# Optimization experiments

Hardware: AMD Instinct MI355X
Metric: run time of the kernel (lower is better)

## Reference

```python
import jax, jax.numpy as jnp
import numpy as np

B, S, E, H, W = 1, 4096, 1024, 16, 256
D = E // H
SCALE = D ** -0.5


def setup_inputs() -> dict:
    key = jax.random.key(0)
    k1, k2, k3 = jax.random.split(key, 3)
    x = jax.random.normal(k1, (B, S, E), dtype=jnp.float32)
    # torch Linear weight is [out,in]; we store transposed [in,out] so y = x @ w
    w_qkv = jax.random.normal(k2, (E, 3 * E), dtype=jnp.float32) * (E ** -0.5)
    w_out = jax.random.normal(k3, (E, E), dtype=jnp.float32) * (E ** -0.5)
    # sliding-window causal mask: key j allowed for query i iff i-W < j <= i
    q_idx = jnp.arange(S)[:, None]
    k_idx = jnp.arange(S)[None, :]
    allowed_mask = (k_idx <= q_idx) & (k_idx > q_idx - W)  # [S,S] bool
    allowed_mask = allowed_mask[None, None]  # [1,1,S,S]
    return {"x": x, "allowed_mask": allowed_mask, "w_qkv": w_qkv, "w_out": w_out}


def reference(x, allowed_mask, w_qkv, w_out):
    b, s, e = x.shape
    qkv = (x @ w_qkv).reshape(b, s, 3, H, D)
    q, k, v = jnp.moveaxis(qkv, 2, 0)  # each [b,s,H,D]
    q = q.transpose(0, 2, 1, 3)  # [b,H,s,D]
    k = k.transpose(0, 2, 1, 3)
    v = v.transpose(0, 2, 1, 3)
    scores = jnp.einsum('bhsd,bhtd->bhst', q, k) * SCALE  # [b,H,s,s]
    scores = jnp.where(allowed_mask, scores, -jnp.inf)
    attn = jax.nn.softmax(scores, axis=-1)
    out = jnp.einsum('bhst,bhtd->bhsd', attn, v)  # [b,H,s,D]
    out = out.transpose(0, 2, 1, 3).reshape(b, s, e)
    return out @ w_out
```

## Files before the change

### kernel.cpp

```cpp
#include <hip/hip_runtime.h>
#include <hip/hip_bf16.h>

#define S_LEN 4096
#define EMB   1024
#define NH    16
#define HD    64
#define WIN   256
#define SCALE 0.125f

typedef __attribute__((ext_vector_type(8))) short short8;
typedef __attribute__((ext_vector_type(4))) float f32x4;
typedef __attribute__((ext_vector_type(4))) unsigned short us4;

__device__ inline unsigned short f2b(float x) {
    __hip_bfloat16 b = __float2bfloat16(x);
    return *reinterpret_cast<unsigned short*>(&b);
}

__device__ inline void gld_lds16(const unsigned short* g, unsigned short* l) {
    __builtin_amdgcn_global_load_lds(
        (const __attribute__((address_space(1))) unsigned int*)g,
        (__attribute__((address_space(3))) unsigned int*)l,
        16, 0, 0);
}

__device__ inline void transpose_tile(const float* __restrict__ in,
                                      unsigned short* __restrict__ out,
                                      int R, int C, int bx, int by,
                                      unsigned short* t) {
    const int tid = threadIdx.x;
    const int r0 = by * 64, c0 = bx * 64;

    const int rr = tid >> 4, cc = (tid & 15) * 4;
    #pragma unroll
    for (int i = 0; i < 4; ++i) {
        float4 v = *reinterpret_cast<const float4*>(&in[(size_t)(r0 + rr + i * 16) * C + c0 + cc]);
        t[(cc + 0) * 72 + rr + i * 16] = f2b(v.x);
        t[(cc + 1) * 72 + rr + i * 16] = f2b(v.y);
        t[(cc + 2) * 72 + rr + i * 16] = f2b(v.z);
        t[(cc + 3) * 72 + rr + i * 16] = f2b(v.w);
    }
    __syncthreads();

    const int wr = tid >> 2, wk = (tid & 3) * 16;
    #pragma unroll
    for (int p = 0; p < 2; ++p)
        *reinterpret_cast<uint4*>(&out[(size_t)(c0 + wr) * R + r0 + wk + p * 8]) =
            *reinterpret_cast<const uint4*>(&t[wr * 72 + wk + p * 8]);
}

__global__ __launch_bounds__(256) void prep(const float* __restrict__ x,
                                            unsigned short* __restrict__ xb,
                                            const float* __restrict__ w_qkv,
                                            unsigned short* __restrict__ wqkvT,
                                            const float* __restrict__ w_out,
                                            unsigned short* __restrict__ woutT) {
    __shared__ alignas(16) unsigned short t[64 * 72];
    const int b = blockIdx.x;
    if (b < 768) {
        transpose_tile(w_qkv, wqkvT, EMB, 3 * EMB, b % 48, b / 48, t);
    } else if (b < 1024) {
        const int bb = b - 768;
        transpose_tile(w_out, woutT, EMB, EMB, bb & 15, bb >> 4, t);
    } else {
        const size_t tt = (size_t)(b - 1024) * 256 + threadIdx.x;
        const float4* s4 = reinterpret_cast<const float4*>(x) + tt * 4;
        float4 v0 = s4[0], v1 = s4[1], v2 = s4[2], v3 = s4[3];
        us4 p0 = {f2b(v0.x), f2b(v0.y), f2b(v0.z), f2b(v0.w)};
        us4 p1 = {f2b(v1.x), f2b(v1.y), f2b(v1.z), f2b(v1.w)};
        us4 p2 = {f2b(v2.x), f2b(v2.y), f2b(v2.z), f2b(v2.w)};
        us4 p3 = {f2b(v3.x), f2b(v3.y), f2b(v3.z), f2b(v3.w)};
        us4* d = reinterpret_cast<us4*>(xb) + tt * 4;
        d[0] = p0; d[1] = p1; d[2] = p2; d[3] = p3;
    }
}

template <int MODE, int BN>
__global__ __launch_bounds__(256) void gemm_bt(const unsigned short* __restrict__ A,
                                               const unsigned short* __restrict__ Bt,
                                               void* __restrict__ Cout,
                                               unsigned short* __restrict__ vT,
                                               int M, int N, int K) {
    constexpr int SMEM_ELEMS = (MODE == 1) ? 17408 : 8192 + BN * 64;
    constexpr int NJ = BN / 32;
    __shared__ alignas(16) unsigned short smem[SMEM_ELEMS];
    unsigned short* As = smem;
    unsigned short* Bs = smem + 8192;

    const int tid  = threadIdx.x;
    const int lane = tid & 63;
    const int w    = tid >> 6;
    const int quad = lane >> 4;
    const int l16  = lane & 15;

    const int m0 = blockIdx.y * 128;
    const int n0 = blockIdx.x * BN;
    const int m_off = (w & 1) * 64;
    const int n_off = (w >> 1) * (BN / 2);

    const int s_row = tid >> 3;
    const int s_c0  = tid & 7;

    f32x4 acc[4][NJ];
    #pragma unroll
    for (int i = 0; i < 4; ++i)
        #pragma unroll
        for (int j = 0; j < NJ; ++j)
            acc[i][j] = (f32x4){0.f, 0.f, 0.f, 0.f};

    for (int bk = 0; bk < K; bk += 64) {
        __syncthreads();
        #pragma unroll
        for (int p = 0; p < 4; ++p) {
            const int row = p * 32 + s_row;
            const int c   = s_c0 ^ (row & 7);
            gld_lds16(A + (size_t)(m0 + row) * K + bk + c * 8,
                      As + (p * 256 + w * 64) * 8);
        }
        #pragma unroll
        for (int p = 0; p < BN / 32; ++p) {
            const int row = p * 32 + s_row;
            const int c   = s_c0 ^ (row & 7);
            gld_lds16(Bt + (size_t)(n0 + row) * K + bk + c * 8,
                      Bs + (p * 256 + w * 64) * 8);
        }
        __syncthreads();

        #pragma unroll
        for (int ks = 0; ks < 2; ++ks) {
            short8 af[4], bf[NJ];
            #pragma unroll
            for (int i = 0; i < 4; ++i) {
                const int r = m_off + i * 16 + l16;
                af[i] = *reinterpret_cast<const short8*>(
                    &As[r * 64 + ((ks * 4 + quad) ^ (r & 7)) * 8]);
            }
            #pragma unroll
            for (int j = 0; j < NJ; ++j) {
                const int r = n_off + j * 16 + l16;
                bf[j] = *reinterpret_cast<const short8*>(
                    &Bs[r * 64 + ((ks * 4 + quad) ^ (r & 7)) * 8]);
            }
            #pragma unroll
            for (int i = 0; i < 4; ++i)
                #pragma unroll
                for (int j = 0; j < NJ; ++j)
                    acc[i][j] = __builtin_amdgcn_mfma_f32_16x16x32_bf16(
                        af[i], bf[j], acc[i][j], 0, 0, 0);
        }
    }

    if (MODE == 0) {
        float* C = (float*)Cout;
        #pragma unroll
        for (int i = 0; i < 4; ++i)
            #pragma unroll
            for (int r = 0; r < 4; ++r) {
                const size_t row = m0 + m_off + i * 16 + quad * 4 + r;
                #pragma unroll
                for (int j = 0; j < NJ; ++j)
                    C[row * N + n0 + n_off + j * 16 + l16] = acc[i][j][r];
            }
    } else if (n0 < 2048) {
        const float sc = (n0 < 1024) ? SCALE : 1.0f;
        unsigned short* C = (unsigned short*)Cout;
        #pragma unroll
        for (int i = 0; i < 4; ++i)
            #pragma unroll
            for (int r = 0; r < 4; ++r) {
                const size_t row = m0 + m_off + i * 16 + quad * 4 + r;
                #pragma unroll
                for (int j = 0; j < NJ; ++j)
                    C[row * N + n0 + n_off + j * 16 + l16] = f2b(acc[i][j][r] * sc);
            }
    } else {
        __syncthreads();
        #pragma unroll
        for (int i = 0; i < 4; ++i) {
            const int ss = m_off + i * 16 + quad * 4;
            #pragma unroll
            for (int j = 0; j < NJ; ++j) {
                const int dd = n_off + j * 16 + l16;
                us4 pk = {f2b(acc[i][j][0]), f2b(acc[i][j][1]),
                          f2b(acc[i][j][2]), f2b(acc[i][j][3])};
                *reinterpret_cast<us4*>(&smem[dd * 136 + ss]) = pk;
            }
        }
        __syncthreads();
        #pragma unroll
        for (int p = 0; p < 8; ++p) {
            const int t  = p * 256 + tid;
            const int dd = t >> 4;
            const int sc2 = (t & 15) * 8;
            *reinterpret_cast<uint4*>(&vT[(size_t)(n0 - 2048 + dd) * S_LEN + m0 + sc2]) =
                *reinterpret_cast<const uint4*>(&smem[dd * 136 + sc2]);
        }
    }
}

__global__ __launch_bounds__(512) void gemm_qkv(const unsigned short* __restrict__ A,
                                                const unsigned short* __restrict__ Bt,
                                                unsigned short* __restrict__ C,
                                                unsigned short* __restrict__ vT) {
    __shared__ alignas(16) unsigned short smem[65536];

    constexpr int K = EMB;
    const int tid  = threadIdx.x;
    const int lane = tid & 63;
    const int w    = tid >> 6;
    const int quad = lane >> 4;
    const int l16  = lane & 15;
    const int wr   = w >> 2, wc = w & 3;
    const int wm0  = wr * 128, wn0 = wc * 64;

    const int raw = blockIdx.x;
    const int s   = (raw & 7) * 24 + (raw >> 3);
    const int by  = s / 12, bx = s % 12;
    const int m0  = by * 256, n0 = bx * 256;

    const int srow = tid >> 2;
    const int scp  = tid & 3;
    const int sc4  = scp ^ ((srow >> 1) & 3);
    const unsigned short* pA = A  + (size_t)(m0 + srow) * K + sc4 * 8;
    const unsigned short* pB = Bt + (size_t)(n0 + srow) * K + sc4 * 8;
    const int dls = (w * 64) * 8;

    auto STAGE = [&](int q) {
        unsigned short* dA = smem + ((q >> 1) & 1) * 32768 + (q & 1) * 8192 + dls;
        unsigned short* dB = dA + 16384;
        const int gk = q * 32;
        gld_lds16(pA + gk, dA);
        gld_lds16(pA + (size_t)128 * K + gk, dA + 4096);
        gld_lds16(pB + gk, dB);
        gld_lds16(pB + (size_t)128 * K + gk, dB + 4096);
    };

    const int cpf = quad ^ ((l16 >> 1) & 3);
    const int oA  = (wm0 + l16) * 32 + cpf * 8;
    const int oB  = (wn0 + l16) * 32 + cpf * 8;

    f32x4 acc[8][4];
    #pragma unroll
    for (int i = 0; i < 8; ++i)
        #pragma unroll
        for (int j = 0; j < 4; ++j)
            acc[i][j] = (f32x4){0.f, 0.f, 0.f, 0.f};

    auto PHASE = [&](int p, bool stage_ok) {
        const unsigned short* Ab = smem + ((p >> 1) & 1) * 32768 + (p & 1) * 8192;
        const unsigned short* Bb = Ab + 16384;
        short8 af[8], bf[4];
        #pragma unroll
        for (int i = 0; i < 8; ++i)
            af[i] = *reinterpret_cast<const short8*>(&Ab[oA + i * 512]);
        #pragma unroll
        for (int j = 0; j < 4; ++j)
            bf[j] = *reinterpret_cast<const short8*>(&Bb[oB + j * 512]);
        if (stage_ok) STAGE(p + 3);
        __builtin_amdgcn_s_setprio(1);
        #pragma unroll
        for (int i = 0; i < 8; ++i)
            #pragma unroll
            for (int j = 0; j < 4; ++j)
                acc[i][j] = __builtin_amdgcn_mfma_f32_16x16x32_bf16(af[i], bf[j], acc[i][j], 0, 0, 0);
        __builtin_amdgcn_s_setprio(0);
    };

    STAGE(0); STAGE(1); STAGE(2);
    asm volatile("s_waitcnt vmcnt(8)" ::: "memory");
    __builtin_amdgcn_s_barrier();

    for (int pp = 0; pp < 28; pp += 4) {
        #pragma unroll
        for (int e = 0; e < 4; ++e) {
            PHASE(pp + e, true);
            asm volatile("s_waitcnt vmcnt(8)" ::: "memory");
            __builtin_amdgcn_s_barrier();
        }
    }
    PHASE(28, true);
    asm volatile("s_waitcnt vmcnt(8)" ::: "memory");
    __builtin_amdgcn_s_barrier();
    PHASE(29, false);
    asm volatile("s_waitcnt vmcnt(4)" ::: "memory");
    __builtin_amdgcn_s_barrier();
    PHASE(30, false);
    asm volatile("s_waitcnt vmcnt(0)" ::: "memory");
    __builtin_amdgcn_s_barrier();
    PHASE(31, false);
    __builtin_amdgcn_s_barrier();

    const int sec = n0 >> 10;
    if (sec < 2) {
        const float sc = (sec == 0) ? SCALE : 1.0f;
        #pragma unroll
        for (int i = 0; i < 8; ++i) {
            #pragma unroll
            for (int r = 0; r < 4; ++r) {
                const size_t row = (size_t)(m0 + wm0 + i * 16 + quad * 4 + r) * 3072;
                #pragma unroll
                for (int j = 0; j < 4; ++j)
                    C[row + n0 + wn0 + j * 16 + l16] = f2b(acc[i][j][r] * sc);
            }
        }
    } else {
        #pragma unroll
        for (int i = 0; i < 8; ++i) {
            const int ss = wm0 + i * 16 + quad * 4;
            const int sc0 = ss >> 3, se = ss & 7;
            #pragma unroll
            for (int j = 0; j < 4; ++j) {
                const int d = wn0 + j * 16 + l16;
                us4 pk = {f2b(acc[i][j][0]), f2b(acc[i][j][1]),
                          f2b(acc[i][j][2]), f2b(acc[i][j][3])};
                *reinterpret_cast<us4*>(&smem[d * 256 + ((sc0 ^ (d & 31)) << 3) + se]) = pk;
            }
        }
        __builtin_amdgcn_s_barrier();
        const int vb = n0 - 2048;
        #pragma unroll
        for (int rep = 0; rep < 16; ++rep) {
            const int idx = rep * 512 + tid;
            const int d = idx >> 5, scr = idx & 31;
            *reinterpret_cast<uint4*>(&vT[(size_t)(vb + d) * S_LEN + m0 + scr * 8]) =
                *reinterpret_cast<const uint4*>(&smem[d * 256 + ((scr ^ (d & 31)) << 3)]);
        }
    }
}

typedef __attribute__((ext_vector_type(2))) unsigned int u32x2;

template <int PAR>
__device__ __forceinline__ void pv_phase(const u32x2 (&PA)[17], unsigned short* scrw,
                                         const unsigned short* Vt, f32x4 (&acco)[4],
                                         int ks0, int quad, int l16, short8 af) {
    const int wq  = quad & 1;
    const int tlq = quad >> 1;
    #pragma unroll
    for (int ksi = 0; ksi < 9; ++ksi) {
        const int ks = ks0 + ksi;
        if (ksi < 8) {
            #pragma unroll
            for (int tl = 0; tl < 2; ++tl) {
                const int nb = 2 * (ksi + 1) + tl - PAR;
                u32x2 v = (nb >= 0 && nb <= 16) ? PA[(nb < 0) ? 0 : ((nb > 16) ? 16 : nb)]
                                                : (u32x2){0u, 0u};
                *reinterpret_cast<u32x2*>(&scrw[((ksi + 1) & 1) * 768 + tl * 384 + l16 * 24 + quad * 4]) = v;
            }
        }
        const int cc = ks * 4 + quad;
        #pragma unroll
        for (int nb2 = 0; nb2 < 4; ++nb2) {
            const int d    = nb2 * 16 + l16;
            const int vpos = (cc & ~7) | ((cc & 7) ^ (d & 7));
            const short8 bfr = *reinterpret_cast<const short8*>(&Vt[d * 320 + vpos * 8]);
            acco[nb2] = __builtin_amdgcn_mfma_f32_16x16x32_bf16(af, bfr, acco[nb2], 0, 0, 0);
        }
        if (ksi < 8)
            af = *reinterpret_cast<const short8*>(&scrw[((ksi + 1) & 1) * 768 + tlq * 384 + l16 * 24 + wq * 8]);
    }
}

__global__ __launch_bounds__(256, 3) void attn_mfma(const unsigned short* __restrict__ qkv,
                                                    const unsigned short* __restrict__ vT,
                                                    unsigned short* __restrict__ outb) {
    __shared__ alignas(16) unsigned short lds[26624];
    unsigned short* KtV = lds;
    unsigned short* scr = lds + 20480;

    const int raw  = blockIdx.x + (blockIdx.y << 6);
    const int xcd  = raw & 7;
    const int slot = raw >> 3;
    const int q0   = (xcd * 8 + (slot & 7)) * 64;
    const int h    = slot >> 3;

    const int tid  = threadIdx.x;
    const int w    = tid >> 6;
    const int lane = tid & 63;
    const int quad = lane >> 4;
    const int l16  = lane & 15;
    const int kbase = q0 - 256;

    const unsigned short* qrow = qkv + (size_t)(q0 + w * 16 + l16) * 3072 + h * 64;
    short8 aq[2];
    aq[0] = *reinterpret_cast<const short8*>(qrow + quad * 8);
    aq[1] = *reinterpret_cast<const short8*>(qrow + 32 + quad * 8);

    #pragma unroll
    for (int i = 0; i < 10; ++i) {
        const int fc  = i * 256 + tid;
        const int row = fc >> 3, p = fc & 7;
        const int c   = p ^ (row & 7);
        int j = kbase + row; if (j < 0) j = 0;
        gld_lds16(qkv + (size_t)j * 3072 + EMB + h * 64 + c * 8,
                  KtV + (i * 256 + w * 64) * 8);
    }

    __syncthreads();

    const int iq = q0 + w * 16 + l16;
    float rsum = 0.f;
    u32x2 PA[17];
    #pragma unroll
    for (int nb = 0; nb < 17; ++nb) {
        const int row = (w + nb) * 16 + l16;
        f32x4 acc = (f32x4){0.f, 0.f, 0.f, 0.f};
        #pragma unroll
        for (int ks = 0; ks < 2; ++ks) {
            const int p = (ks * 4 + quad) ^ (l16 & 7);
            const short8 kf = *reinterpret_cast<const short8*>(&KtV[row * 64 + p * 8]);
            acc = __builtin_amdgcn_mfma_f32_16x16x32_bf16(kf, aq[ks], acc, 0, 0, 0);
        }
        const int jb = kbase + (w + nb) * 16 + quad * 4;
        float ev0, ev1, ev2, ev3;
        {
            const int j0 = jb, j1 = jb + 1, j2 = jb + 2, j3 = jb + 3;
            ev0 = ((j0 >= 0) & (j0 <= iq) & (j0 > iq - WIN)) ? __expf(acc[0]) : 0.f;
            ev1 = ((j1 >= 0) & (j1 <= iq) & (j1 > iq - WIN)) ? __expf(acc[1]) : 0.f;
            ev2 = ((j2 >= 0) & (j2 <= iq) & (j2 > iq - WIN)) ? __expf(acc[2]) : 0.f;
            ev3 = ((j3 >= 0) & (j3 <= iq) & (j3 > iq - WIN)) ? __expf(acc[3]) : 0.f;
        }
        rsum += (ev0 + ev1) + (ev2 + ev3);
        PA[nb][0] = ((unsigned)f2b(ev1) << 16) | f2b(ev0);
        PA[nb][1] = ((unsigned)f2b(ev3) << 16) | f2b(ev2);
    }
    rsum += __shfl_xor(rsum, 16, 64);
    rsum += __shfl_xor(rsum, 32, 64);
    const float inv_l = 1.f / rsum;

    __syncthreads();

    #pragma unroll
    for (int i = 0; i < 10; ++i) {
        const int fc = i * 256 + tid;
        const int d  = fc / 40, pp = fc % 40;
        const int cc = (pp & ~7) | ((pp & 7) ^ (d & 7));
        int j0 = kbase + cc * 8; if (j0 < 0) j0 = 0;
        gld_lds16(vT + (size_t)(h * 64 + d) * S_LEN + j0,
                  KtV + (i * 256 + w * 64) * 8);
    }

    unsigned short* scrw = scr + w * 1536;
    const int par = w & 1;
    {
        const u32x2 z = {0u, 0u};
        u32x2 v0 = par ? z : PA[0];
        u32x2 v1 = par ? PA[0] : PA[1];
        *reinterpret_cast<u32x2*>(&scrw[0 * 384 + l16 * 24 + quad * 4]) = v0;
        *reinterpret_cast<u32x2*>(&scrw[1 * 384 + l16 * 24 + quad * 4]) = v1;
    }
    const short8 af0 = *reinterpret_cast<const short8*>(
        &scrw[(quad >> 1) * 384 + l16 * 24 + (quad & 1) * 8]);

    __syncthreads();

    f32x4 acco[4];
    #pragma unroll
    for (int nb2 = 0; nb2 < 4; ++nb2) acco[nb2] = (f32x4){0.f, 0.f, 0.f, 0.f};

    const int ks0 = w >> 1;
    if (par == 0) pv_phase<0>(PA, scrw, KtV, acco, ks0, quad, l16, af0);
    else          pv_phase<1>(PA, scrw, KtV, acco, ks0, quad, l16, af0);

    float invo[4];
    #pragma unroll
    for (int r = 0; r < 4; ++r)
        invo[r] = __shfl(inv_l, quad * 4 + r, 64);

    #pragma unroll
    for (int nb2 = 0; nb2 < 4; ++nb2)
        #pragma unroll
        for (int r = 0; r < 4; ++r)
            outb[(size_t)(q0 + w * 16 + quad * 4 + r) * EMB + h * 64 + nb2 * 16 + l16] =
                f2b(acco[nb2][r] * invo[r]);
}

extern "C" void kernel_launch(void* const* d_in, const int* in_sizes, int n_in,
                              void* d_out, int out_size, void* d_ws, size_t ws_size,
                              hipStream_t stream) {
    const float* x     = (const float*)d_in[0];
    const float* w_qkv = (const float*)d_in[2];
    const float* w_out = (const float*)d_in[3];
    float* out = (float*)d_out;

    char* ws = (char*)d_ws;
    unsigned short* xb     = (unsigned short*)(ws);
    unsigned short* wqkvT  = (unsigned short*)(ws + (8u  << 20));
    unsigned short* woutT  = (unsigned short*)(ws + (14u << 20));
    unsigned short* qkvb   = (unsigned short*)(ws + (16u << 20));
    unsigned short* attnb  = (unsigned short*)(ws + (48u << 20));
    unsigned short* vT     = (unsigned short*)(ws + (56u << 20));

    prep<<<2048, 256, 0, stream>>>(x, xb, w_qkv, wqkvT, w_out, woutT);

    gemm_qkv<<<dim3(192), 512, 0, stream>>>(xb, wqkvT, qkvb, vT);

    attn_mfma<<<dim3(S_LEN / 64, NH), 256, 0, stream>>>(qkvb, vT, attnb);

    gemm_bt<0, 64><<<dim3(EMB / 64, S_LEN / 128), 256, 0, stream>>>(
        attnb, woutT, out, nullptr, S_LEN, EMB, EMB);
}
```

Measured before the change: 182.0 us.

## Double-buffer A fragments in registers and prefetch next phase during MFMAs

Restructures the QKV GEMM main loop so the A-operand LDS fragments for the next k-phase are loaded into a second register set while the current phase's MFMAs run, ping-ponging between two register arrays. Wait counts are tightened from vmcnt(8) to vmcnt(4) so the next stage's LDS data is resident before the early read. MFMA loop order is swapped to iterate j outer, i inner. This aims to hide LDS read latency behind matrix math, at the cost of 32 more VGPRs for the extra fragments, which may reduce occupancy, and a shallower effective global-load pipeline.

```diff
diff --git a/kernel.cpp b/kernel.cpp
--- a/kernel.cpp
+++ b/kernel.cpp
@@ -235,6 +235,10 @@
         gld_lds16(pB + (size_t)128 * K + gk, dB + 4096);
     };
 
+    auto BASE = [&](int p) -> const unsigned short* {
+        return smem + ((p >> 1) & 1) * 32768 + (p & 1) * 8192;
+    };
+
     const int cpf = quad ^ ((l16 >> 1) & 3);
     const int oA  = (wm0 + l16) * 32 + cpf * 8;
     const int oB  = (wn0 + l16) * 32 + cpf * 8;
@@ -246,49 +250,61 @@
         for (int j = 0; j < 4; ++j)
             acc[i][j] = (f32x4){0.f, 0.f, 0.f, 0.f};
 
-    auto PHASE = [&](int p, bool stage_ok) {
-        const unsigned short* Ab = smem + ((p >> 1) & 1) * 32768 + (p & 1) * 8192;
-        const unsigned short* Bb = Ab + 16384;
-        short8 af[8], bf[4];
-        #pragma unroll
-        for (int i = 0; i < 8; ++i)
-            af[i] = *reinterpret_cast<const short8*>(&Ab[oA + i * 512]);
-        #pragma unroll
-        for (int j = 0; j < 4; ++j)
-            bf[j] = *reinterpret_cast<const short8*>(&Bb[oB + j * 512]);
-        if (stage_ok) STAGE(p + 3);
-        __builtin_amdgcn_s_setprio(1);
-        #pragma unroll
-        for (int i = 0; i < 8; ++i)
-            #pragma unroll
-            for (int j = 0; j < 4; ++j)
-                acc[i][j] = __builtin_amdgcn_mfma_f32_16x16x32_bf16(af[i], bf[j], acc[i][j], 0, 0, 0);
-        __builtin_amdgcn_s_setprio(0);
-    };
+    short8 afA[8], afB[8];
+
+#define PHASE_RR(p, CUR, NXT, DO_PF, DO_ST) do {                               \
+    const unsigned short* Bb_ = BASE(p) + 16384;                               \
+    short8 bf[4];                                                              \
+    _Pragma("unroll")                                                          \
+    for (int j = 0; j < 4; ++j)                                                \
+        bf[j] = *reinterpret_cast<const short8*>(&Bb_[oB + j * 512]);          \
+    if (DO_PF) {                                                               \
+        const unsigned short* An_ = BASE((p) + 1);                             \
+        _Pragma("unroll")                                                      \
+        for (int i = 0; i < 8; ++i)                                            \
+            NXT[i] = *reinterpret_cast<const short8*>(&An_[oA + i * 512]);     \
+    }                                                                          \
+    if (DO_ST) STAGE((p) + 3);                                                 \
+    __builtin_amdgcn_s_setprio(1);                                             \
+    _Pragma("unroll")                                                          \
+    for (int j = 0; j < 4; ++j)                                                \
+        _Pragma("unroll")                                                      \
+        for (int i = 0; i < 8; ++i)                                            \
+            acc[i][j] = __builtin_amdgcn_mfma_f32_16x16x32_bf16(               \
+                CUR[i], bf[j], acc[i][j], 0, 0, 0);                            \
+    __builtin_amdgcn_s_setprio(0);                                             \
+} while (0)
 
     STAGE(0); STAGE(1); STAGE(2);
-    asm volatile("s_waitcnt vmcnt(8)" ::: "memory");
-    __builtin_amdgcn_s_barrier();
-
-    for (int pp = 0; pp < 28; pp += 4) {
-        #pragma unroll
-        for (int e = 0; e < 4; ++e) {
-            PHASE(pp + e, true);
-            asm volatile("s_waitcnt vmcnt(8)" ::: "memory");
-            __builtin_amdgcn_s_barrier();
-        }
-    }
-    PHASE(28, true);
-    asm volatile("s_waitcnt vmcnt(8)" ::: "memory");
-    __builtin_amdgcn_s_barrier();
-    PHASE(29, false);
     asm volatile("s_waitcnt vmcnt(4)" ::: "memory");
     __builtin_amdgcn_s_barrier();
-    PHASE(30, false);
+    {
+        const unsigned short* A0_ = BASE(0);
+        #pragma unroll
+        for (int i = 0; i < 8; ++i)
+            afA[i] = *reinterpret_cast<const short8*>(&A0_[oA + i * 512]);
+    }
+
+    for (int pp = 0; pp < 28; pp += 2) {
+        PHASE_RR(pp, afA, afB, true, true);
+        asm volatile("s_waitcnt vmcnt(4)" ::: "memory");
+        __builtin_amdgcn_s_barrier();
+        PHASE_RR(pp + 1, afB, afA, true, true);
+        asm volatile("s_waitcnt vmcnt(4)" ::: "memory");
+        __builtin_amdgcn_s_barrier();
+    }
+    PHASE_RR(28, afA, afB, true, true);
+    asm volatile("s_waitcnt vmcnt(4)" ::: "memory");
+    __builtin_amdgcn_s_barrier();
+    PHASE_RR(29, afB, afA, true, false);
     asm volatile("s_waitcnt vmcnt(0)" ::: "memory");
     __builtin_amdgcn_s_barrier();
-    PHASE(31, false);
+    PHASE_RR(30, afA, afB, true, false);
     __builtin_amdgcn_s_barrier();
+    PHASE_RR(31, afB, afA, false, false);
+    __builtin_amdgcn_s_barrier();
+
+#undef PHASE_RR
 
     const int sec = n0 >> 10;
     if (sec < 2) {
```

New measurement: 181.7 us. About the same (-0.2%).
